# Optimization experiments

Hardware: AMD Instinct MI355X
Metric: run time of the kernel (lower is better)

Reference implementation:

```python
import jax, jax.numpy as jnp
import numpy as np

BLOCK = 32  # ggml quant block size


def setup_inputs() -> dict:
    key = jax.random.key(0)
    k1, k2, k3, k4 = jax.random.split(key, 4)
    IN, OUT = 8192, 8192
    x = jax.random.normal(k1, (2, 8, IN), dtype=jnp.float32)
    # quantized codes in [0, 255), centered by -127 at dequant time
    qweight = jax.random.randint(k2, (OUT, IN), 0, 255, dtype=jnp.int32)
    # per-block scales, small positive values like real ggml d
    scales = jax.random.uniform(k3, (OUT, IN // BLOCK), dtype=jnp.float32) * 0.01
    bias = jax.random.normal(k4, (OUT,), dtype=jnp.float32)
    return {"x": x, "qweight": qweight, "scales": scales, "bias": bias}


def reference(x, qweight, scales, bias):
    OUT, IN = qweight.shape
    # dequantize: centered int codes * per-block scale -> [OUT, IN]
    w = (qweight.astype(jnp.float32) - 127.0).reshape(OUT, IN // BLOCK, BLOCK)
    w = (w * scales[:, :, None]).reshape(OUT, IN)
    xf = x.reshape(-1, IN)                     # [T, IN]
    out = xf @ w.T + bias                      # [T, OUT]
    return out.reshape(*x.shape[:-1], OUT)
```

## Files before the change

kernel.cpp:

```cpp
#include <hip/hip_runtime.h>
#include <stdint.h>

#define INF 8192
#define OUTF 8192
#define TOK 16
#define KSPLIT 8
#define KR (INF / KSPLIT)
#define NI (KR / 32)
#define ROWS_PER_BLOCK 64
#define LDS_STRIDE (KR + 8)

typedef __attribute__((ext_vector_type(8))) short short8;
typedef __attribute__((ext_vector_type(4))) short short4v;
typedef __attribute__((ext_vector_type(4))) float float4v;
typedef __attribute__((ext_vector_type(4))) int int4v;
typedef __attribute__((ext_vector_type(4))) uint32_t uint4v;

__device__ __forceinline__ short f2bf(float f) {
    uint32_t u = __builtin_bit_cast(uint32_t, f);
    u += 0x7fffu + ((u >> 16) & 1u);
    return (short)(u >> 16);
}

__device__ __forceinline__ uint32_t pkbf(float a, float b) {
    uint32_t ua = __builtin_bit_cast(uint32_t, a) + 0x8000u;
    uint32_t ub = __builtin_bit_cast(uint32_t, b) + 0x8000u;
    return (ua >> 16) | (ub & 0xffff0000u);
}

__device__ __forceinline__ void stage_x(const float* __restrict__ x, short* xs,
                                        int k0, int tid) {
    #pragma unroll
    for (int it = 0; it < (TOK * KR / 4) / 256; ++it) {
        int idx = tid + it * 256;
        int t  = idx >> 8;
        int kq = idx & 255;
        float4v xv = *reinterpret_cast<const float4v*>(x + (size_t)t * INF + k0 + kq * 4);
        short4v h;
        h[0] = f2bf(xv[0]); h[1] = f2bf(xv[1]); h[2] = f2bf(xv[2]); h[3] = f2bf(xv[3]);
        *reinterpret_cast<short4v*>(xs + t * LDS_STRIDE + kq * 4) = h;
    }
}

__device__ __forceinline__ float4v kloop(const short* xs,
                                         const int* __restrict__ qrow,
                                         const float* __restrict__ srow,
                                         int lane, float4v acc) {
    int col = lane & 15;
    int kg  = lane >> 4;
    const short* aptr = xs + col * LDS_STRIDE + kg * 8;

    int4v A0 = *reinterpret_cast<const int4v*>(qrow);
    int4v B0 = *reinterpret_cast<const int4v*>(qrow + 4);
    int4v A1 = *reinterpret_cast<const int4v*>(qrow + 32);
    int4v B1 = *reinterpret_cast<const int4v*>(qrow + 36);
    float s0 = srow[0], s1 = srow[1];

    #pragma unroll 4
    for (int i = 0; i < NI; ++i) {
        int ip = (i + 2 < NI) ? (i + 2) : (NI - 1);
        int4v A2 = *reinterpret_cast<const int4v*>(qrow + ip * 32);
        int4v B2 = *reinterpret_cast<const int4v*>(qrow + ip * 32 + 4);
        float s2 = srow[ip];

        float m = -127.0f * s0;
        float f0 = fmaf((float)A0[0], s0, m);
        float f1 = fmaf((float)A0[1], s0, m);
        float f2 = fmaf((float)A0[2], s0, m);
        float f3 = fmaf((float)A0[3], s0, m);
        float f4 = fmaf((float)B0[0], s0, m);
        float f5 = fmaf((float)B0[1], s0, m);
        float f6 = fmaf((float)B0[2], s0, m);
        float f7 = fmaf((float)B0[3], s0, m);

        uint4v pk;
        pk[0] = pkbf(f0, f1);
        pk[1] = pkbf(f2, f3);
        pk[2] = pkbf(f4, f5);
        pk[3] = pkbf(f6, f7);
        short8 bfrag = __builtin_bit_cast(short8, pk);

        short8 afrag = *reinterpret_cast<const short8*>(aptr + i * 32);

        acc = __builtin_amdgcn_mfma_f32_16x16x32_bf16(afrag, bfrag, acc, 0, 0, 0);

        A0 = A1; B0 = B1; s0 = s1;
        A1 = A2; B1 = B2; s1 = s2;
    }
    return acc;
}

__global__ __launch_bounds__(256, 4) void gemm_q8_part(
    const float* __restrict__ x, const int* __restrict__ qw,
    const float* __restrict__ scales, float* __restrict__ pbuf)
{
    __shared__ short xs[TOK * LDS_STRIDE];
    int rg = blockIdx.x >> 3;
    int ks = blockIdx.x & 7;
    int k0 = ks * KR;
    int tid = threadIdx.x;

    stage_x(x, xs, k0, tid);
    __syncthreads();

    int wave = tid >> 6;
    int lane = tid & 63;
    int col  = lane & 15;
    int kg   = lane >> 4;
    int r0 = rg * ROWS_PER_BLOCK + wave * 16;
    int r  = r0 + col;

    const int*   qrow = qw + (size_t)r * INF + k0 + kg * 8;
    const float* srow = scales + (size_t)r * (INF / 32) + (k0 >> 5);

    float4v acc = {0.f, 0.f, 0.f, 0.f};
    acc = kloop(xs, qrow, srow, lane, acc);

    float* pb = pbuf + (size_t)ks * TOK * OUTF;
    #pragma unroll
    for (int i = 0; i < 4; ++i) {
        int t = kg * 4 + i;
        pb[(size_t)t * OUTF + r0 + col] = acc[i];
    }
}

__global__ __launch_bounds__(256) void reduce_bias_k(
    const float* __restrict__ pbuf, const float* __restrict__ bias,
    float* __restrict__ out)
{
    int gid = blockIdx.x * 256 + threadIdx.x;
    int f = gid * 4;
    int t = f >> 13;
    int r = f & (OUTF - 1);
    float4v a = *reinterpret_cast<const float4v*>(bias + r);
    #pragma unroll
    for (int s = 0; s < KSPLIT; ++s) {
        float4v p = *reinterpret_cast<const float4v*>(pbuf + (size_t)(s * TOK + t) * OUTF + r);
        a += p;
    }
    *reinterpret_cast<float4v*>(out + f) = a;
}

__global__ __launch_bounds__(256, 4) void gemm_q8_direct(
    const float* __restrict__ x, const int* __restrict__ qw,
    const float* __restrict__ scales, const float* __restrict__ bias,
    float* __restrict__ out)
{
    __shared__ short xs[TOK * LDS_STRIDE];
    int rg = blockIdx.x;
    int tid = threadIdx.x;
    int wave = tid >> 6;
    int lane = tid & 63;
    int col  = lane & 15;
    int kg   = lane >> 4;
    int r0 = rg * ROWS_PER_BLOCK + wave * 16;
    int r  = r0 + col;

    float4v acc = {0.f, 0.f, 0.f, 0.f};
    for (int ks = 0; ks < KSPLIT; ++ks) {
        int k0 = ks * KR;
        __syncthreads();
        stage_x(x, xs, k0, tid);
        __syncthreads();
        const int*   qrow = qw + (size_t)r * INF + k0 + kg * 8;
        const float* srow = scales + (size_t)r * (INF / 32) + (k0 >> 5);
        acc = kloop(xs, qrow, srow, lane, acc);
    }
    #pragma unroll
    for (int i = 0; i < 4; ++i) {
        int t = kg * 4 + i;
        out[(size_t)t * OUTF + r0 + col] = acc[i] + bias[r0 + col];
    }
}

extern "C" void kernel_launch(void* const* d_in, const int* in_sizes, int n_in,
                              void* d_out, int out_size, void* d_ws, size_t ws_size,
                              hipStream_t stream) {
    const float* x      = (const float*)d_in[0];
    const int*   qw     = (const int*)d_in[1];
    const float* scales = (const float*)d_in[2];
    const float* bias   = (const float*)d_in[3];
    float* out = (float*)d_out;

    size_t need = (size_t)KSPLIT * TOK * OUTF * sizeof(float);
    if (ws_size >= need) {
        float* pbuf = (float*)d_ws;
        gemm_q8_part<<<(OUTF / ROWS_PER_BLOCK) * KSPLIT, 256, 0, stream>>>(x, qw, scales, pbuf);
        reduce_bias_k<<<(TOK * OUTF / 4) / 256, 256, 0, stream>>>(pbuf, bias, out);
    } else {
        gemm_q8_direct<<<OUTF / ROWS_PER_BLOCK, 256, 0, stream>>>(x, qw, scales, bias, out);
    }
}
```

Before: 56.82 us.

## Replace split-K two-kernel GEMM with single-pass in-block K reduction

Drops the global split-K partial buffer and the separate reduce kernel. Each 512-thread block now covers 16 output rows, and its 8 waves each take one K slice. Partial sums are reduced through shared memory, and bias is added in the same kernel. x is read straight from global memory and converted to bf16 in registers, replacing the LDS staging. This removes one launch and the partial-sum write and read traffic. In exchange, every wave rereads x from global memory or cache, and 256 threads idle during the final reduction.

```diff
diff --git a/kernel.cpp b/kernel.cpp
--- a/kernel.cpp
+++ b/kernel.cpp
@@ -4,23 +4,15 @@
 #define INF 8192
 #define OUTF 8192
 #define TOK 16
-#define KSPLIT 8
-#define KR (INF / KSPLIT)
+#define NWAVE 8
+#define KR (INF / NWAVE)
 #define NI (KR / 32)
-#define ROWS_PER_BLOCK 64
-#define LDS_STRIDE (KR + 8)
+#define NRG (OUTF / 16)
 
 typedef __attribute__((ext_vector_type(8))) short short8;
-typedef __attribute__((ext_vector_type(4))) short short4v;
 typedef __attribute__((ext_vector_type(4))) float float4v;
 typedef __attribute__((ext_vector_type(4))) int int4v;
 typedef __attribute__((ext_vector_type(4))) uint32_t uint4v;
-
-__device__ __forceinline__ short f2bf(float f) {
-    uint32_t u = __builtin_bit_cast(uint32_t, f);
-    u += 0x7fffu + ((u >> 16) & 1u);
-    return (short)(u >> 16);
-}
 
 __device__ __forceinline__ uint32_t pkbf(float a, float b) {
     uint32_t ua = __builtin_bit_cast(uint32_t, a) + 0x8000u;
@@ -28,148 +20,88 @@
     return (ua >> 16) | (ub & 0xffff0000u);
 }
 
-__device__ __forceinline__ void stage_x(const float* __restrict__ x, short* xs,
-                                        int k0, int tid) {
-    #pragma unroll
-    for (int it = 0; it < (TOK * KR / 4) / 256; ++it) {
-        int idx = tid + it * 256;
-        int t  = idx >> 8;
-        int kq = idx & 255;
-        float4v xv = *reinterpret_cast<const float4v*>(x + (size_t)t * INF + k0 + kq * 4);
-        short4v h;
-        h[0] = f2bf(xv[0]); h[1] = f2bf(xv[1]); h[2] = f2bf(xv[2]); h[3] = f2bf(xv[3]);
-        *reinterpret_cast<short4v*>(xs + t * LDS_STRIDE + kq * 4) = h;
-    }
+__device__ __forceinline__ short8 dequant8(int4v A, int4v B, float s) {
+    float m = -127.0f * s;
+    uint4v pk;
+    pk[0] = pkbf(fmaf((float)A[0], s, m), fmaf((float)A[1], s, m));
+    pk[1] = pkbf(fmaf((float)A[2], s, m), fmaf((float)A[3], s, m));
+    pk[2] = pkbf(fmaf((float)B[0], s, m), fmaf((float)B[1], s, m));
+    pk[3] = pkbf(fmaf((float)B[2], s, m), fmaf((float)B[3], s, m));
+    return __builtin_bit_cast(short8, pk);
 }
 
-__device__ __forceinline__ float4v kloop(const short* xs,
-                                         const int* __restrict__ qrow,
-                                         const float* __restrict__ srow,
-                                         int lane, float4v acc) {
-    int col = lane & 15;
-    int kg  = lane >> 4;
-    const short* aptr = xs + col * LDS_STRIDE + kg * 8;
+__device__ __forceinline__ short8 packx(float4v a, float4v b) {
+    uint4v pk;
+    pk[0] = pkbf(a[0], a[1]);
+    pk[1] = pkbf(a[2], a[3]);
+    pk[2] = pkbf(b[0], b[1]);
+    pk[3] = pkbf(b[2], b[3]);
+    return __builtin_bit_cast(short8, pk);
+}
 
-    int4v A0 = *reinterpret_cast<const int4v*>(qrow);
-    int4v B0 = *reinterpret_cast<const int4v*>(qrow + 4);
-    int4v A1 = *reinterpret_cast<const int4v*>(qrow + 32);
-    int4v B1 = *reinterpret_cast<const int4v*>(qrow + 36);
-    float s0 = srow[0], s1 = srow[1];
+__global__ __launch_bounds__(512, 4) void gemm_q8_onepass(
+    const float* __restrict__ x, const int* __restrict__ qw,
+    const float* __restrict__ scales, const float* __restrict__ bias,
+    float* __restrict__ out)
+{
+    __shared__ float red[NWAVE * 256];
+    int tid  = threadIdx.x;
+    int wave = tid >> 6;
+    int lane = tid & 63;
+    int col  = lane & 15;
+    int kg   = lane >> 4;
+    int rg   = blockIdx.x;
+    int r0   = rg * 16;
+    int r    = r0 + col;
+    int k0   = wave * KR;
+
+    const int*   qrow = qw + (size_t)r * INF + k0 + kg * 8;
+    const float* srow = scales + (size_t)r * (INF / 32) + (k0 >> 5);
+    const float* xrow = x + (size_t)col * INF + k0 + kg * 8;
+
+    int4v  A0 = *reinterpret_cast<const int4v*>(qrow);
+    int4v  B0 = *reinterpret_cast<const int4v*>(qrow + 4);
+    int4v  A1 = *reinterpret_cast<const int4v*>(qrow + 32);
+    int4v  B1 = *reinterpret_cast<const int4v*>(qrow + 36);
+    float  s0 = srow[0], s1 = srow[1];
+    float4v XA0 = *reinterpret_cast<const float4v*>(xrow);
+    float4v XB0 = *reinterpret_cast<const float4v*>(xrow + 4);
+    float4v XA1 = *reinterpret_cast<const float4v*>(xrow + 32);
+    float4v XB1 = *reinterpret_cast<const float4v*>(xrow + 36);
+
+    float4v acc = {0.f, 0.f, 0.f, 0.f};
 
     #pragma unroll 4
     for (int i = 0; i < NI; ++i) {
         int ip = (i + 2 < NI) ? (i + 2) : (NI - 1);
-        int4v A2 = *reinterpret_cast<const int4v*>(qrow + ip * 32);
-        int4v B2 = *reinterpret_cast<const int4v*>(qrow + ip * 32 + 4);
-        float s2 = srow[ip];
+        int4v  A2 = *reinterpret_cast<const int4v*>(qrow + ip * 32);
+        int4v  B2 = *reinterpret_cast<const int4v*>(qrow + ip * 32 + 4);
+        float  s2 = srow[ip];
+        float4v XA2 = *reinterpret_cast<const float4v*>(xrow + ip * 32);
+        float4v XB2 = *reinterpret_cast<const float4v*>(xrow + ip * 32 + 4);
 
-        float m = -127.0f * s0;
-        float f0 = fmaf((float)A0[0], s0, m);
-        float f1 = fmaf((float)A0[1], s0, m);
-        float f2 = fmaf((float)A0[2], s0, m);
-        float f3 = fmaf((float)A0[3], s0, m);
-        float f4 = fmaf((float)B0[0], s0, m);
-        float f5 = fmaf((float)B0[1], s0, m);
-        float f6 = fmaf((float)B0[2], s0, m);
-        float f7 = fmaf((float)B0[3], s0, m);
-
-        uint4v pk;
-        pk[0] = pkbf(f0, f1);
-        pk[1] = pkbf(f2, f3);
-        pk[2] = pkbf(f4, f5);
-        pk[3] = pkbf(f6, f7);
-        short8 bfrag = __builtin_bit_cast(short8, pk);
-
-        short8 afrag = *reinterpret_cast<const short8*>(aptr + i * 32);
+        short8 bfrag = dequant8(A0, B0, s0);
+        short8 afrag = packx(XA0, XB0);
 
         acc = __builtin_amdgcn_mfma_f32_16x16x32_bf16(afrag, bfrag, acc, 0, 0, 0);
 
-        A0 = A1; B0 = B1; s0 = s1;
-        A1 = A2; B1 = B2; s1 = s2;
+        A0 = A1;  B0 = B1;  s0 = s1;  XA0 = XA1;  XB0 = XB1;
+        A1 = A2;  B1 = B2;  s1 = s2;  XA1 = XA2;  XB1 = XB2;
     }
-    return acc;
-}
 
-__global__ __launch_bounds__(256, 4) void gemm_q8_part(
-    const float* __restrict__ x, const int* __restrict__ qw,
-    const float* __restrict__ scales, float* __restrict__ pbuf)
-{
-    __shared__ short xs[TOK * LDS_STRIDE];
-    int rg = blockIdx.x >> 3;
-    int ks = blockIdx.x & 7;
-    int k0 = ks * KR;
-    int tid = threadIdx.x;
-
-    stage_x(x, xs, k0, tid);
+    *reinterpret_cast<float4v*>(&red[wave * 256 + lane * 4]) = acc;
     __syncthreads();
 
-    int wave = tid >> 6;
-    int lane = tid & 63;
-    int col  = lane & 15;
-    int kg   = lane >> 4;
-    int r0 = rg * ROWS_PER_BLOCK + wave * 16;
-    int r  = r0 + col;
-
-    const int*   qrow = qw + (size_t)r * INF + k0 + kg * 8;
-    const float* srow = scales + (size_t)r * (INF / 32) + (k0 >> 5);
-
-    float4v acc = {0.f, 0.f, 0.f, 0.f};
-    acc = kloop(xs, qrow, srow, lane, acc);
-
-    float* pb = pbuf + (size_t)ks * TOK * OUTF;
-    #pragma unroll
-    for (int i = 0; i < 4; ++i) {
-        int t = kg * 4 + i;
-        pb[(size_t)t * OUTF + r0 + col] = acc[i];
-    }
-}
-
-__global__ __launch_bounds__(256) void reduce_bias_k(
-    const float* __restrict__ pbuf, const float* __restrict__ bias,
-    float* __restrict__ out)
-{
-    int gid = blockIdx.x * 256 + threadIdx.x;
-    int f = gid * 4;
-    int t = f >> 13;
-    int r = f & (OUTF - 1);
-    float4v a = *reinterpret_cast<const float4v*>(bias + r);
-    #pragma unroll
-    for (int s = 0; s < KSPLIT; ++s) {
-        float4v p = *reinterpret_cast<const float4v*>(pbuf + (size_t)(s * TOK + t) * OUTF + r);
-        a += p;
-    }
-    *reinterpret_cast<float4v*>(out + f) = a;
-}
-
-__global__ __launch_bounds__(256, 4) void gemm_q8_direct(
-    const float* __restrict__ x, const int* __restrict__ qw,
-    const float* __restrict__ scales, const float* __restrict__ bias,
-    float* __restrict__ out)
-{
-    __shared__ short xs[TOK * LDS_STRIDE];
-    int rg = blockIdx.x;
-    int tid = threadIdx.x;
-    int wave = tid >> 6;
-    int lane = tid & 63;
-    int col  = lane & 15;
-    int kg   = lane >> 4;
-    int r0 = rg * ROWS_PER_BLOCK + wave * 16;
-    int r  = r0 + col;
-
-    float4v acc = {0.f, 0.f, 0.f, 0.f};
-    for (int ks = 0; ks < KSPLIT; ++ks) {
-        int k0 = ks * KR;
-        __syncthreads();
-        stage_x(x, xs, k0, tid);
-        __syncthreads();
-        const int*   qrow = qw + (size_t)r * INF + k0 + kg * 8;
-        const float* srow = scales + (size_t)r * (INF / 32) + (k0 >> 5);
-        acc = kloop(xs, qrow, srow, lane, acc);
-    }
-    #pragma unroll
-    for (int i = 0; i < 4; ++i) {
-        int t = kg * 4 + i;
-        out[(size_t)t * OUTF + r0 + col] = acc[i] + bias[r0 + col];
+    if (tid < 256) {
+        int t  = tid >> 4;
+        int rc = tid & 15;
+        int l  = (t >> 2) * 16 + rc;
+        int m  = t & 3;
+        float a = bias[r0 + rc];
+        #pragma unroll
+        for (int w = 0; w < NWAVE; ++w)
+            a += red[w * 256 + l * 4 + m];
+        out[(size_t)t * OUTF + r0 + rc] = a;
     }
 }
 
@@ -182,12 +114,5 @@
     const float* bias   = (const float*)d_in[3];
     float* out = (float*)d_out;
 
-    size_t need = (size_t)KSPLIT * TOK * OUTF * sizeof(float);
-    if (ws_size >= need) {
-        float* pbuf = (float*)d_ws;
-        gemm_q8_part<<<(OUTF / ROWS_PER_BLOCK) * KSPLIT, 256, 0, stream>>>(x, qw, scales, pbuf);
-        reduce_bias_k<<<(TOK * OUTF / 4) / 256, 256, 0, stream>>>(pbuf, bias, out);
-    } else {
-        gemm_q8_direct<<<OUTF / ROWS_PER_BLOCK, 256, 0, stream>>>(x, qw, scales, bias, out);
-    }
+    gemm_q8_onepass<<<NRG, 512, 0, stream>>>(x, qw, scales, bias, out);
 }
```

Result: slower. 79.49 us (+39.9%).
